# Kernel tuning notes

Measured on AMD Instinct MI355X. Metric: run time of the kernel, lower is better.

## Reference

```python
import jax, jax.numpy as jnp
import numpy as np

N_NODES = 100000
N_EDGES = 1600000
D = 64


def setup_inputs() -> dict:
    key = jax.random.key(0)
    k0, k1, k2, k3 = jax.random.split(key, 4)
    x = jax.random.normal(k0, (N_NODES, D), dtype=jnp.float32)
    edge_index = jax.random.randint(k1, (2, N_EDGES), 0, N_NODES, dtype=jnp.int64)
    W1 = jax.random.normal(k2, (D, D), dtype=jnp.float32) * 0.1
    b1 = jnp.zeros((D,), dtype=jnp.float32)
    W2 = jax.random.normal(k3, (D, D), dtype=jnp.float32) * 0.1
    b2 = jnp.zeros((D,), dtype=jnp.float32)
    return {"x": x, "edge_index": edge_index, "W1": W1, "b1": b1, "W2": W2, "b2": b2}


def _gcn_layer(x, edge_index, W, b):
    n = x.shape[0]
    h = x @ W  # [N, Dout] -- transform before aggregation (small GEMM)
    loop = jnp.arange(n, dtype=edge_index.dtype)
    src = jnp.concatenate([edge_index[0], loop])
    dst = jnp.concatenate([edge_index[1], loop])
    deg = jax.ops.segment_sum(jnp.ones_like(dst, dtype=h.dtype), dst, num_segments=n)
    dinv = jax.lax.rsqrt(deg)  # deg >= 1 thanks to self loops
    norm = dinv[src] * dinv[dst]  # [E+N]
    msg = h[src] * norm[:, None]  # gather: [E+N, Dout]
    agg = jax.ops.segment_sum(msg, dst, num_segments=n)  # scatter-add
    return agg + b


def reference(x, edge_index, W1, b1, W2, b2):
    # dropout p = 0.0 -> identity
    h = jax.nn.relu(_gcn_layer(x, edge_index, W1, b1))
    h = jax.nn.relu(_gcn_layer(h, edge_index, W2, b2))
    return h
```

## Files before the change

kernel.cpp:

```cpp
#include <hip/hip_runtime.h>
#include <hip/hip_bf16.h>

#define D 64
#define NB_HIST 256
#define MAXBK 512

typedef float vfloat4 __attribute__((ext_vector_type(4)));

__device__ __forceinline__ unsigned short f2bf(float f) {
    union { float f; unsigned u; } v; v.f = f;
    unsigned r = (v.u + 0x7FFF + ((v.u >> 16) & 1)) >> 16;
    return (unsigned short)r;
}
__device__ __forceinline__ float bflo(unsigned u) {
    union { unsigned u; float f; } v; v.u = u << 16; return v.f;
}
__device__ __forceinline__ float bfhi(unsigned u) {
    union { unsigned u; float f; } v; v.u = u & 0xFFFF0000u; return v.f;
}

__global__ __launch_bounds__(256) void passA_gemm(
    const int* __restrict__ dst, int* __restrict__ blockCounts, int E, int per, int NBK,
    const float* __restrict__ X, const float* __restrict__ W,
    unsigned short* __restrict__ hn, int N)
{
    int tid = threadIdx.x;

    if ((int)blockIdx.x < NB_HIST) {
        __shared__ int hist[MAXBK];
        for (int i = tid; i < NBK; i += 256) hist[i] = 0;
        __syncthreads();
        int lo = blockIdx.x * per, hi = min(E, lo + per);
        for (int i = lo + tid * 4; i < hi; i += 1024) {
            if (i + 3 < hi) {
                int4 d4 = *(const int4*)(dst + i);
                atomicAdd(&hist[d4.x >> 8], 1);
                atomicAdd(&hist[d4.y >> 8], 1);
                atomicAdd(&hist[d4.z >> 8], 1);
                atomicAdd(&hist[d4.w >> 8], 1);
            } else {
                for (int k = i; k < hi; ++k) atomicAdd(&hist[dst[k] >> 8], 1);
            }
        }
        __syncthreads();
        for (int i = tid; i < NBK; i += 256)
            blockCounts[(size_t)blockIdx.x * NBK + i] = hist[i];
        return;
    }

    __shared__ float sW[D * D];
    __shared__ float sX[32 * D];
    int rowBase = ((int)blockIdx.x - NB_HIST) * 32;

    for (int i = tid; i < 1024; i += 256)
        ((vfloat4*)sW)[i] = ((const vfloat4*)W)[i];
    for (int i = tid; i < 512; i += 256) {
        int r = rowBase + (i >> 4);
        vfloat4 v = (vfloat4)0.0f;
        if (r < N) v = __builtin_nontemporal_load(((const vfloat4*)X) + rowBase * 16 + i);
        ((vfloat4*)sX)[i] = v;
    }
    __syncthreads();

    int wave = tid >> 6, lane = tid & 63;
    float accv[8];
#pragma unroll
    for (int r = 0; r < 8; ++r) accv[r] = 0.0f;
    int xoff = (wave * 8) * D;
#pragma unroll 8
    for (int k = 0; k < D; ++k) {
        float wv = sW[k * D + lane];
#pragma unroll
        for (int r = 0; r < 8; ++r)
            accv[r] += sX[xoff + r * D + k] * wv;
    }
#pragma unroll
    for (int r = 0; r < 8; ++r) {
        int row = rowBase + wave * 8 + r;
        if (row < N) hn[(size_t)row * D + lane] = f2bf(accv[r]);
    }
}

__global__ __launch_bounds__(256) void scan_cols(
    const int* __restrict__ blockCounts, int* __restrict__ partial,
    int* __restrict__ totals, int NBK)
{
    int wave = threadIdx.x >> 6, lane = threadIdx.x & 63;
    int k = blockIdx.x * 4 + wave;
    if (k >= NBK) return;
    int carry = 0;
    for (int base = 0; base < NB_HIST; base += 64) {
        int b = base + lane;
        int v = blockCounts[(size_t)b * NBK + k];
        int inc = v;
        for (int d = 1; d < 64; d <<= 1) {
            int t = __shfl_up(inc, d, 64);
            if (lane >= d) inc += t;
        }
        partial[(size_t)k * NB_HIST + b] = inc - v + carry;
        carry += __shfl(inc, 63, 64);
    }
    if (lane == 0) totals[k] = carry;
}

__global__ void scan_buckets(const int* __restrict__ totals, int* __restrict__ bofs, int NBK) {
    int lane = threadIdx.x;
    int carry = 0;
    for (int base = 0; base < NBK; base += 64) {
        int i = base + lane;
        int v = (i < NBK) ? totals[i] : 0;
        int inc = v;
        for (int d = 1; d < 64; d <<= 1) {
            int t = __shfl_up(inc, d, 64);
            if (lane >= d) inc += t;
        }
        if (i < NBK) bofs[i] = inc - v + carry;
        carry += __shfl(inc, 63, 64);
    }
}

__global__ __launch_bounds__(256) void passB(
    const int* __restrict__ src, const int* __restrict__ dst,
    const int* __restrict__ bofs, const int* __restrict__ partial,
    int* __restrict__ bucketed, int E, int per, int NBK)
{
    __shared__ int cur[MAXBK];
    int tid = threadIdx.x, b = blockIdx.x;
    for (int i = tid; i < NBK; i += 256)
        cur[i] = bofs[i] + partial[(size_t)i * NB_HIST + b];
    __syncthreads();
    int lo = b * per, hi = min(E, lo + per);
    for (int i = lo + tid * 4; i < hi; i += 1024) {
        if (i + 3 < hi) {
            int4 d4 = *(const int4*)(dst + i);
            int4 s4 = *(const int4*)(src + i);
            int p0 = atomicAdd(&cur[d4.x >> 8], 1);
            int p1 = atomicAdd(&cur[d4.y >> 8], 1);
            int p2 = atomicAdd(&cur[d4.z >> 8], 1);
            int p3 = atomicAdd(&cur[d4.w >> 8], 1);
            bucketed[p0] = (s4.x << 8) | (d4.x & 255);
            bucketed[p1] = (s4.y << 8) | (d4.y & 255);
            bucketed[p2] = (s4.z << 8) | (d4.z & 255);
            bucketed[p3] = (s4.w << 8) | (d4.w & 255);
        } else {
            for (int k = i; k < hi; ++k) {
                int d = dst[k], s = src[k];
                int pos = atomicAdd(&cur[d >> 8], 1);
                bucketed[pos] = (s << 8) | (d & 255);
            }
        }
    }
}

__global__ __launch_bounds__(256) void build_csr_scale(
    const int* __restrict__ bucketed, const int* __restrict__ bofs,
    const int* __restrict__ totals, int* __restrict__ deg, float* __restrict__ dinv,
    int* __restrict__ ofs, int* __restrict__ csr,
    unsigned short* __restrict__ hn, int N)
{
    __shared__ int h[256];
    __shared__ int scn[256];
    __shared__ float sdv[256];
    int tid = threadIdx.x, k = blockIdx.x;
    int e0 = bofs[k], e1 = e0 + totals[k];
    int node = k * 256 + tid;

    h[tid] = 0;
    __syncthreads();
    for (int i = e0 + tid; i < e1; i += 256)
        atomicAdd(&h[bucketed[i] & 255], 1);
    __syncthreads();

    int mydeg = h[tid];
    scn[tid] = mydeg;
    __syncthreads();
    for (int d2 = 1; d2 < 256; d2 <<= 1) {
        int t = (tid >= d2) ? scn[tid - d2] : 0;
        __syncthreads();
        scn[tid] += t;
        __syncthreads();
    }
    int myofs = scn[tid] - mydeg;

    float dv = rsqrtf((float)(mydeg + 1));
    sdv[tid] = dv;
    if (node < N) {
        deg[node]  = mydeg;
        dinv[node] = dv;
        ofs[node]  = e0 + myofs;
    }

    h[tid] = myofs;
    __syncthreads();
    for (int i = e0 + tid; i < e1; i += 256) {
        int v = bucketed[i];
        int pos = atomicAdd(&h[v & 255], 1);
        csr[e0 + pos] = v >> 8;
    }

    __syncthreads();
    int4* hp = (int4*)hn;
    for (int c = tid; c < 2048; c += 256) {
        int r = c >> 3;
        int n2 = k * 256 + r;
        if (n2 < N) {
            float f = sdv[r];
            size_t idx = (size_t)n2 * 8 + (c & 7);
            int4 hv = hp[idx];
            unsigned r0 = (unsigned)f2bf(bflo(hv.x) * f) | ((unsigned)f2bf(bfhi(hv.x) * f) << 16);
            unsigned r1 = (unsigned)f2bf(bflo(hv.y) * f) | ((unsigned)f2bf(bfhi(hv.y) * f) << 16);
            unsigned r2 = (unsigned)f2bf(bflo(hv.z) * f) | ((unsigned)f2bf(bfhi(hv.z) * f) << 16);
            unsigned r3 = (unsigned)f2bf(bflo(hv.w) * f) | ((unsigned)f2bf(bfhi(hv.w) * f) << 16);
            hp[idx] = make_int4((int)r0, (int)r1, (int)r2, (int)r3);
        }
    }
}

__global__ __launch_bounds__(256) void gemm2(
    const unsigned short* __restrict__ h1b, const float* __restrict__ W,
    const float* __restrict__ dinv, unsigned short* __restrict__ hn, int N)
{
    __shared__ float sW[D * D];
    __shared__ float sX[32 * D];
    int tid = threadIdx.x;
    int rowBase = blockIdx.x * 32;

    for (int i = tid; i < 1024; i += 256)
        ((vfloat4*)sW)[i] = ((const vfloat4*)W)[i];
    {
        int r = tid >> 3, c8 = tid & 7;
        int row = rowBase + r;
        int4 hv = make_int4(0, 0, 0, 0);
        if (row < N) hv = ((const int4*)h1b)[(size_t)row * 8 + c8];
        float* dst8 = &sX[r * D + c8 * 8];
        dst8[0] = bflo(hv.x); dst8[1] = bfhi(hv.x);
        dst8[2] = bflo(hv.y); dst8[3] = bfhi(hv.y);
        dst8[4] = bflo(hv.z); dst8[5] = bfhi(hv.z);
        dst8[6] = bflo(hv.w); dst8[7] = bfhi(hv.w);
    }
    __syncthreads();

    int wave = tid >> 6, lane = tid & 63;
    float accv[8];
#pragma unroll
    for (int r = 0; r < 8; ++r) accv[r] = 0.0f;
    int xoff = (wave * 8) * D;
#pragma unroll 8
    for (int k = 0; k < D; ++k) {
        float wv = sW[k * D + lane];
#pragma unroll
        for (int r = 0; r < 8; ++r)
            accv[r] += sX[xoff + r * D + k] * wv;
    }
#pragma unroll
    for (int r = 0; r < 8; ++r) {
        int row = rowBase + wave * 8 + r;
        if (row < N) hn[(size_t)row * D + lane] = f2bf(accv[r] * dinv[row]);
    }
}

template <bool BF16OUT>
__global__ __launch_bounds__(256) void aggregate_relu(
    const int* __restrict__ ofs, const int* __restrict__ deg,
    const int* __restrict__ csr, const unsigned short* __restrict__ hn,
    const float* __restrict__ dinv, const float* __restrict__ bias,
    void* __restrict__ outv, int N)
{
    int t    = blockIdx.x * 256 + threadIdx.x;
    int lane = threadIdx.x & 63;
    int grp  = lane >> 3, sub = lane & 7;
    int node = (t >> 6) * 8 + grp;
    bool live = (node < N);

    const int4* hrow = (const int4*)hn;
    float2 a0 = {0.f, 0.f}, a1 = {0.f, 0.f}, a2 = {0.f, 0.f}, a3 = {0.f, 0.f};

    int s0 = 0, cnt = 0;
    if (live) {
        s0  = ofs[node];
        cnt = deg[node];
        int4 h = hrow[(size_t)node * 8 + sub];
        a0.x += bflo(h.x); a0.y += bfhi(h.x);
        a1.x += bflo(h.y); a1.y += bfhi(h.y);
        a2.x += bflo(h.z); a2.y += bfhi(h.z);
        a3.x += bflo(h.w); a3.y += bfhi(h.w);
    }

    const int* cp = csr + s0;
    int j = 0;
    for (; j + 3 < cnt; j += 4) {
        int sA = cp[j], sB = cp[j + 1], sC = cp[j + 2], sD = cp[j + 3];
        int4 hA = hrow[(size_t)sA * 8 + sub];
        int4 hB = hrow[(size_t)sB * 8 + sub];
        int4 hC = hrow[(size_t)sC * 8 + sub];
        int4 hD = hrow[(size_t)sD * 8 + sub];
        a0.x += bflo(hA.x); a0.y += bfhi(hA.x);
        a1.x += bflo(hA.y); a1.y += bfhi(hA.y);
        a2.x += bflo(hA.z); a2.y += bfhi(hA.z);
        a3.x += bflo(hA.w); a3.y += bfhi(hA.w);
        a0.x += bflo(hB.x); a0.y += bfhi(hB.x);
        a1.x += bflo(hB.y); a1.y += bfhi(hB.y);
        a2.x += bflo(hB.z); a2.y += bfhi(hB.z);
        a3.x += bflo(hB.w); a3.y += bfhi(hB.w);
        a0.x += bflo(hC.x); a0.y += bfhi(hC.x);
        a1.x += bflo(hC.y); a1.y += bfhi(hC.y);
        a2.x += bflo(hC.z); a2.y += bfhi(hC.z);
        a3.x += bflo(hC.w); a3.y += bfhi(hC.w);
        a0.x += bflo(hD.x); a0.y += bfhi(hD.x);
        a1.x += bflo(hD.y); a1.y += bfhi(hD.y);
        a2.x += bflo(hD.z); a2.y += bfhi(hD.z);
        a3.x += bflo(hD.w); a3.y += bfhi(hD.w);
    }
    for (; j < cnt; ++j) {
        int sA = cp[j];
        int4 hA = hrow[(size_t)sA * 8 + sub];
        a0.x += bflo(hA.x); a0.y += bfhi(hA.x);
        a1.x += bflo(hA.y); a1.y += bfhi(hA.y);
        a2.x += bflo(hA.z); a2.y += bfhi(hA.z);
        a3.x += bflo(hA.w); a3.y += bfhi(hA.w);
    }

    if (live) {
        float dw = dinv[node];
        float4 b0 = ((const float4*)bias)[sub * 2];
        float4 b1 = ((const float4*)bias)[sub * 2 + 1];
        float o0 = fmaxf(a0.x * dw + b0.x, 0.f);
        float o1 = fmaxf(a0.y * dw + b0.y, 0.f);
        float o2 = fmaxf(a1.x * dw + b0.z, 0.f);
        float o3 = fmaxf(a1.y * dw + b0.w, 0.f);
        float o4 = fmaxf(a2.x * dw + b1.x, 0.f);
        float o5 = fmaxf(a2.y * dw + b1.y, 0.f);
        float o6 = fmaxf(a3.x * dw + b1.z, 0.f);
        float o7 = fmaxf(a3.y * dw + b1.w, 0.f);
        if (BF16OUT) {
            unsigned r0 = (unsigned)f2bf(o0) | ((unsigned)f2bf(o1) << 16);
            unsigned r1 = (unsigned)f2bf(o2) | ((unsigned)f2bf(o3) << 16);
            unsigned r2 = (unsigned)f2bf(o4) | ((unsigned)f2bf(o5) << 16);
            unsigned r3 = (unsigned)f2bf(o6) | ((unsigned)f2bf(o7) << 16);
            ((int4*)outv)[(size_t)node * 8 + sub] =
                make_int4((int)r0, (int)r1, (int)r2, (int)r3);
        } else {
            float4 v0 = make_float4(o0, o1, o2, o3);
            float4 v1 = make_float4(o4, o5, o6, o7);
            ((float4*)outv)[(size_t)node * 16 + sub * 2]     = v0;
            ((float4*)outv)[(size_t)node * 16 + sub * 2 + 1] = v1;
        }
    }
}


extern "C" void kernel_launch(void* const* d_in, const int* in_sizes, int n_in,
                              void* d_out, int out_size, void* d_ws, size_t ws_size,
                              hipStream_t stream) {
    const float* x   = (const float*)d_in[0];
    const int*   ei  = (const int*)d_in[1];
    const float* W1  = (const float*)d_in[2];
    const float* b1  = (const float*)d_in[3];
    const float* W2  = (const float*)d_in[4];
    const float* b2  = (const float*)d_in[5];

    int N = in_sizes[0] / D;
    int E = in_sizes[1] / 2;
    const int* src = ei;
    const int* dst = ei + E;
    int NBK = (N + 255) >> 8;
    int per = (((E + NB_HIST - 1) / NB_HIST) + 3) & ~3;

    char* ws = (char*)d_ws;
    int*            blockCounts = (int*)(ws + 0x00000000);
    int*            partial     = (int*)(ws + 0x00080000);
    int*            totals      = (int*)(ws + 0x00100000);
    int*            bofs        = (int*)(ws + 0x00110000);
    int*            deg         = (int*)(ws + 0x00120000);
    float*          dinv        = (float*)(ws + 0x00190000);
    int*            ofs         = (int*)(ws + 0x00200000);
    int*            bucketed    = (int*)(ws + 0x00280000);
    int*            csr         = (int*)(ws + 0x00A00000);
    unsigned short* hn          = (unsigned short*)(ws + 0x01100000);
    unsigned short* h1b         = (unsigned short*)(ws + 0x01D80000);
    float*          outF        = (float*)d_out;

    int nb_G = (N + 31) / 32;
    int nb_A = (N + 31) / 32;

    passA_gemm<<<NB_HIST + nb_G, 256, 0, stream>>>(dst, blockCounts, E, per, NBK, x, W1, hn, N);
    scan_cols<<<(NBK + 3) / 4, 256, 0, stream>>>(blockCounts, partial, totals, NBK);
    scan_buckets<<<1, 64, 0, stream>>>(totals, bofs, NBK);
    passB<<<NB_HIST, 256, 0, stream>>>(src, dst, bofs, partial, bucketed, E, per, NBK);
    build_csr_scale<<<NBK, 256, 0, stream>>>(bucketed, bofs, totals, deg, dinv, ofs, csr, hn, N);

    aggregate_relu<true><<<nb_A, 256, 0, stream>>>(ofs, deg, csr, hn, dinv, b1, (void*)h1b, N);
    gemm2<<<nb_G, 256, 0, stream>>>(h1b, W2, dinv, hn, N);
    aggregate_relu<false><<<nb_A, 256, 0, stream>>>(ofs, deg, csr, hn, dinv, b2, (void*)outF, N);
}
```

Baseline: 239.6 us.

## Move both dense transforms to bf16 MFMA with split-precision weights

Replaces the LDS-based FP32 scalar GEMMs for both layers with MFMA 16x16x32 bf16 kernels. Weights are split into high and low bf16 parts (and X for layer 1) to recover near-FP32 accuracy with three or two MFMA passes. Weight fragments are precomputed by extra blocks in the histogram kernel, and gemm1 becomes a separate launch instead of sharing a grid with the histogram. This costs one more launch and the loss of overlap between the histogram and the GEMM.

```diff
diff --git a/kernel.cpp b/kernel.cpp
--- a/kernel.cpp
+++ b/kernel.cpp
@@ -6,12 +6,21 @@
 #define MAXBK 512
 
 typedef float vfloat4 __attribute__((ext_vector_type(4)));
+typedef short short8 __attribute__((ext_vector_type(8)));
+typedef float f32x4 __attribute__((ext_vector_type(4)));
 
 __device__ __forceinline__ unsigned short f2bf(float f) {
     union { float f; unsigned u; } v; v.f = f;
     unsigned r = (v.u + 0x7FFF + ((v.u >> 16) & 1)) >> 16;
     return (unsigned short)r;
 }
+__device__ __forceinline__ unsigned short bftrunc(float f) {
+    union { float f; unsigned u; } v; v.f = f;
+    return (unsigned short)(v.u >> 16);
+}
+__device__ __forceinline__ float bffrom(unsigned short h) {
+    union { unsigned u; float f; } v; v.u = ((unsigned)h) << 16; return v.f;
+}
 __device__ __forceinline__ float bflo(unsigned u) {
     union { unsigned u; float f; } v; v.u = u << 16; return v.f;
 }
@@ -19,10 +28,11 @@
     union { unsigned u; float f; } v; v.u = u & 0xFFFF0000u; return v.f;
 }
 
-__global__ __launch_bounds__(256) void passA_gemm(
+__global__ __launch_bounds__(256) void passA_hist_wfrag(
     const int* __restrict__ dst, int* __restrict__ blockCounts, int E, int per, int NBK,
-    const float* __restrict__ X, const float* __restrict__ W,
-    unsigned short* __restrict__ hn, int N)
+    const float* __restrict__ W1, const float* __restrict__ W2,
+    unsigned short* __restrict__ WfH1, unsigned short* __restrict__ WfL1,
+    unsigned short* __restrict__ WfH2, unsigned short* __restrict__ WfL2)
 {
     int tid = threadIdx.x;
 
@@ -48,36 +58,79 @@
         return;
     }
 
-    __shared__ float sW[D * D];
-    __shared__ float sX[32 * D];
-    int rowBase = ((int)blockIdx.x - NB_HIST) * 32;
-
-    for (int i = tid; i < 1024; i += 256)
-        ((vfloat4*)sW)[i] = ((const vfloat4*)W)[i];
-    for (int i = tid; i < 512; i += 256) {
-        int r = rowBase + (i >> 4);
-        vfloat4 v = (vfloat4)0.0f;
-        if (r < N) v = __builtin_nontemporal_load(((const vfloat4*)X) + rowBase * 16 + i);
-        ((vfloat4*)sX)[i] = v;
-    }
-    __syncthreads();
-
-    int wave = tid >> 6, lane = tid & 63;
-    float accv[8];
-#pragma unroll
-    for (int r = 0; r < 8; ++r) accv[r] = 0.0f;
-    int xoff = (wave * 8) * D;
-#pragma unroll 8
-    for (int k = 0; k < D; ++k) {
-        float wv = sW[k * D + lane];
-#pragma unroll
-        for (int r = 0; r < 8; ++r)
-            accv[r] += sX[xoff + r * D + k] * wv;
-    }
-#pragma unroll
-    for (int r = 0; r < 8; ++r) {
-        int row = rowBase + wave * 8 + r;
-        if (row < N) hn[(size_t)row * D + lane] = f2bf(accv[r]);
+    int b = (int)blockIdx.x - NB_HIST;
+    const float* Wsrc = (b >> 1) ? W2 : W1;
+    unsigned short* fh = (b >> 1) ? WfH2 : WfH1;
+    unsigned short* fl = (b >> 1) ? WfL2 : WfL1;
+    int combo = (b & 1) * 4 + (tid >> 6);
+    int lane = tid & 63;
+    int s = combo >> 2, c = combo & 3, g = lane >> 4, rl = lane & 15;
+#pragma unroll
+    for (int j = 0; j < 8; ++j) {
+        float v = Wsrc[(32 * s + 8 * g + j) * D + 16 * c + rl];
+        unsigned short h = bftrunc(v);
+        fh[combo * 512 + lane * 8 + j] = h;
+        fl[combo * 512 + lane * 8 + j] = f2bf(v - bffrom(h));
+    }
+}
+
+__global__ __launch_bounds__(256) void gemm1_mfma(
+    const float* __restrict__ X,
+    const unsigned short* __restrict__ WfH, const unsigned short* __restrict__ WfL,
+    unsigned short* __restrict__ hn, int N)
+{
+    int t = threadIdx.x, wave = t >> 6, lane = t & 63;
+    int rowBase = (int)blockIdx.x * 64 + wave * 16;
+    if (rowBase >= N) return;
+    int g = lane >> 4, rl = lane & 15;
+
+    short8 BH[2][4], BL[2][4];
+#pragma unroll
+    for (int s = 0; s < 2; ++s)
+#pragma unroll
+        for (int c = 0; c < 4; ++c) {
+            BH[s][c] = *(const short8*)(WfH + ((s * 4 + c) * 64 + lane) * 8);
+            BL[s][c] = *(const short8*)(WfL + ((s * 4 + c) * 64 + lane) * 8);
+        }
+
+    int arow = rowBase + rl; if (arow >= N) arow = N - 1;
+    const float* xr = X + (size_t)arow * D;
+
+    f32x4 acc[4];
+#pragma unroll
+    for (int c = 0; c < 4; ++c) acc[c] = (f32x4){0.f, 0.f, 0.f, 0.f};
+
+#pragma unroll
+    for (int s = 0; s < 2; ++s) {
+        vfloat4 x0 = *(const vfloat4*)(xr + 32 * s + 8 * g);
+        vfloat4 x1 = *(const vfloat4*)(xr + 32 * s + 8 * g + 4);
+        short8 ah, al;
+#pragma unroll
+        for (int j = 0; j < 4; ++j) {
+            unsigned short h0 = bftrunc(x0[j]);
+            ah[j] = (short)h0; al[j] = (short)f2bf(x0[j] - bffrom(h0));
+            unsigned short h1 = bftrunc(x1[j]);
+            ah[j + 4] = (short)h1; al[j + 4] = (short)f2bf(x1[j] - bffrom(h1));
+        }
+#pragma unroll
+        for (int c = 0; c < 4; ++c)
+            acc[c] = __builtin_amdgcn_mfma_f32_16x16x32_bf16(ah, BH[s][c], acc[c], 0, 0, 0);
+#pragma unroll
+        for (int c = 0; c < 4; ++c)
+            acc[c] = __builtin_amdgcn_mfma_f32_16x16x32_bf16(ah, BL[s][c], acc[c], 0, 0, 0);
+#pragma unroll
+        for (int c = 0; c < 4; ++c)
+            acc[c] = __builtin_amdgcn_mfma_f32_16x16x32_bf16(al, BH[s][c], acc[c], 0, 0, 0);
+    }
+
+#pragma unroll
+    for (int r = 0; r < 4; ++r) {
+        int row = rowBase + g * 4 + r;
+        if (row < N) {
+            unsigned short* hr = hn + (size_t)row * D + rl;
+#pragma unroll
+            for (int c = 0; c < 4; ++c) hr[c * 16] = f2bf(acc[c][r]);
+        }
     }
 }
 
@@ -216,46 +269,52 @@
     }
 }
 
-__global__ __launch_bounds__(256) void gemm2(
-    const unsigned short* __restrict__ h1b, const float* __restrict__ W,
+__global__ __launch_bounds__(256) void gemm2_mfma(
+    const unsigned short* __restrict__ h1b,
+    const unsigned short* __restrict__ WfH, const unsigned short* __restrict__ WfL,
     const float* __restrict__ dinv, unsigned short* __restrict__ hn, int N)
 {
-    __shared__ float sW[D * D];
-    __shared__ float sX[32 * D];
-    int tid = threadIdx.x;
-    int rowBase = blockIdx.x * 32;
-
-    for (int i = tid; i < 1024; i += 256)
-        ((vfloat4*)sW)[i] = ((const vfloat4*)W)[i];
-    {
-        int r = tid >> 3, c8 = tid & 7;
-        int row = rowBase + r;
-        int4 hv = make_int4(0, 0, 0, 0);
-        if (row < N) hv = ((const int4*)h1b)[(size_t)row * 8 + c8];
-        float* dst8 = &sX[r * D + c8 * 8];
-        dst8[0] = bflo(hv.x); dst8[1] = bfhi(hv.x);
-        dst8[2] = bflo(hv.y); dst8[3] = bfhi(hv.y);
-        dst8[4] = bflo(hv.z); dst8[5] = bfhi(hv.z);
-        dst8[6] = bflo(hv.w); dst8[7] = bfhi(hv.w);
-    }
-    __syncthreads();
-
-    int wave = tid >> 6, lane = tid & 63;
-    float accv[8];
-#pragma unroll
-    for (int r = 0; r < 8; ++r) accv[r] = 0.0f;
-    int xoff = (wave * 8) * D;
-#pragma unroll 8
-    for (int k = 0; k < D; ++k) {
-        float wv = sW[k * D + lane];
-#pragma unroll
-        for (int r = 0; r < 8; ++r)
-            accv[r] += sX[xoff + r * D + k] * wv;
-    }
-#pragma unroll
-    for (int r = 0; r < 8; ++r) {
-        int row = rowBase + wave * 8 + r;
-        if (row < N) hn[(size_t)row * D + lane] = f2bf(accv[r] * dinv[row]);
+    int t = threadIdx.x, wave = t >> 6, lane = t & 63;
+    int rowBase = (int)blockIdx.x * 64 + wave * 16;
+    if (rowBase >= N) return;
+    int g = lane >> 4, rl = lane & 15;
+
+    short8 BH[2][4], BL[2][4];
+#pragma unroll
+    for (int s = 0; s < 2; ++s)
+#pragma unroll
+        for (int c = 0; c < 4; ++c) {
+            BH[s][c] = *(const short8*)(WfH + ((s * 4 + c) * 64 + lane) * 8);
+            BL[s][c] = *(const short8*)(WfL + ((s * 4 + c) * 64 + lane) * 8);
+        }
+
+    int arow = rowBase + rl; if (arow >= N) arow = N - 1;
+    const unsigned short* hr0 = h1b + (size_t)arow * D;
+
+    f32x4 acc[4];
+#pragma unroll
+    for (int c = 0; c < 4; ++c) acc[c] = (f32x4){0.f, 0.f, 0.f, 0.f};
+
+#pragma unroll
+    for (int s = 0; s < 2; ++s) {
+        short8 a = *(const short8*)(hr0 + 32 * s + 8 * g);
+#pragma unroll
+        for (int c = 0; c < 4; ++c)
+            acc[c] = __builtin_amdgcn_mfma_f32_16x16x32_bf16(a, BH[s][c], acc[c], 0, 0, 0);
+#pragma unroll
+        for (int c = 0; c < 4; ++c)
+            acc[c] = __builtin_amdgcn_mfma_f32_16x16x32_bf16(a, BL[s][c], acc[c], 0, 0, 0);
+    }
+
+#pragma unroll
+    for (int r = 0; r < 4; ++r) {
+        int row = rowBase + g * 4 + r;
+        if (row < N) {
+            float dv = dinv[row];
+            unsigned short* hw = hn + (size_t)row * D + rl;
+#pragma unroll
+            for (int c = 0; c < 4; ++c) hw[c * 16] = f2bf(acc[c][r] * dv);
+        }
     }
 }
 
@@ -378,18 +437,24 @@
     int*            csr         = (int*)(ws + 0x00A00000);
     unsigned short* hn          = (unsigned short*)(ws + 0x01100000);
     unsigned short* h1b         = (unsigned short*)(ws + 0x01D80000);
+    unsigned short* WfH1        = (unsigned short*)(ws + 0x02A80000);
+    unsigned short* WfL1        = WfH1 + 4096;
+    unsigned short* WfH2        = WfL1 + 4096;
+    unsigned short* WfL2        = WfH2 + 4096;
     float*          outF        = (float*)d_out;
 
-    int nb_G = (N + 31) / 32;
+    int nb_G = (N + 63) / 64;
     int nb_A = (N + 31) / 32;
 
-    passA_gemm<<<NB_HIST + nb_G, 256, 0, stream>>>(dst, blockCounts, E, per, NBK, x, W1, hn, N);
+    passA_hist_wfrag<<<NB_HIST + 4, 256, 0, stream>>>(dst, blockCounts, E, per, NBK,
+                                                      W1, W2, WfH1, WfL1, WfH2, WfL2);
+    gemm1_mfma<<<nb_G, 256, 0, stream>>>(x, WfH1, WfL1, hn, N);
     scan_cols<<<(NBK + 3) / 4, 256, 0, stream>>>(blockCounts, partial, totals, NBK);
     scan_buckets<<<1, 64, 0, stream>>>(totals, bofs, NBK);
     passB<<<NB_HIST, 256, 0, stream>>>(src, dst, bofs, partial, bucketed, E, per, NBK);
     build_csr_scale<<<NBK, 256, 0, stream>>>(bucketed, bofs, totals, deg, dinv, ofs, csr, hn, N);
 
     aggregate_relu<true><<<nb_A, 256, 0, stream>>>(ofs, deg, csr, hn, dinv, b1, (void*)h1b, N);
-    gemm2<<<nb_G, 256, 0, stream>>>(h1b, W2, dinv, hn, N);
+    gemm2_mfma<<<nb_G, 256, 0, stream>>>(h1b, WfH2, WfL2, dinv, hn, N);
     aggregate_relu<false><<<nb_A, 256, 0, stream>>>(ofs, deg, csr, hn, dinv, b2, (void*)outF, N);
 }
```

Result: faster. 221.8 us (-7.4%).
